# Kernel optimization log

Measured on AMD Instinct MI355X. Metric: run time of the kernel, lower is better.

The kernel has to match this reference:

```python
import jax, jax.numpy as jnp
import numpy as np


def setup_inputs() -> dict:
    key = jax.random.key(0)
    ks = jax.random.split(key, 6)
    B, Nu, Ni, D = 256, 512, 512, 64
    u_fea = jax.random.normal(ks[0], (B, Nu, D), dtype=jnp.float32)
    i_fea = jax.random.normal(ks[1], (B, Ni, D), dtype=jnp.float32)
    M = jax.random.normal(ks[2], (D, D), dtype=jnp.float32)
    # Linear weights, torch-style: y = x @ W.T + b (init scaled like torch default)
    lim = 1.0 / np.sqrt(D)
    Wu = jax.random.uniform(ks[3], (D, D), minval=-lim, maxval=lim, dtype=jnp.float32)
    Wi = jax.random.uniform(ks[4], (D, D), minval=-lim, maxval=lim, dtype=jnp.float32)
    bu = jnp.zeros((D,), dtype=jnp.float32)
    bi = jnp.zeros((D,), dtype=jnp.float32)
    return {"u_fea": u_fea, "i_fea": i_fea, "M": M, "Wu": Wu, "bu": bu, "Wi": Wi, "bi": bi}


def reference(u_fea, i_fea, M, Wu, bu, Wi, bi):
    # fc_u / fc_i: torch Linear is x @ W.T + b
    u = jnp.einsum('bud,ed->bue', u_fea, Wu) + bu   # [B, Nu, D]
    i = jnp.einsum('bid,ed->bie', i_fea, Wi) + bi   # [B, Ni, D]
    # Bilinear co-attention score S = u @ M @ i^T  -> [B, Nu, Ni]
    uM = jnp.einsum('bud,de->bue', u, M)
    S = jnp.einsum('bue,bie->bui', uM, i)
    # pooling == 'max'
    u_score = S.max(axis=2)   # [B, Nu]
    i_score = S.max(axis=1)   # [B, Ni]
    # gumbel == False -> plain softmax over the review axis
    p_u = jax.nn.softmax(u_score, axis=1)
    p_i = jax.nn.softmax(i_score, axis=1)
    return (p_u[:, :, None], p_i[:, :, None])
```

## Files before the change

kernel.cpp:

```cpp
#include <hip/hip_runtime.h>
#include <hip/hip_bf16.h>
#include <float.h>


#define NBATCH 256
#define NSEQ   512
#define DIM    64

typedef __attribute__((ext_vector_type(8))) short short8;
typedef __attribute__((ext_vector_type(4))) float f32x4;

#define MFMA16(a,b,c) __builtin_amdgcn_mfma_f32_16x16x32_bf16(a,b,c,0,0,0)

union BF2 { __hip_bfloat162 b; short2 s; };

__device__ __forceinline__ void cvt2(float f, unsigned short &h, unsigned short &l) {
    unsigned u = __float_as_uint(f);
    unsigned hb = (u + 0x7FFFu + ((u >> 16) & 1u)) >> 16;
    h = (unsigned short)hb;
    float r = f - __uint_as_float(hb << 16);
    unsigned u2 = __float_as_uint(r);
    l = (unsigned short)((u2 + 0x7FFFu + ((u2 >> 16) & 1u)) >> 16);
}

__device__ __forceinline__ void cvt8(const f32x4 a, const f32x4 b, short8 &hi, short8 &lo) {
    BF2 h0, h1, h2, h3;
    h0.b = __float22bfloat162_rn(make_float2(a[0], a[1]));
    h1.b = __float22bfloat162_rn(make_float2(a[2], a[3]));
    h2.b = __float22bfloat162_rn(make_float2(b[0], b[1]));
    h3.b = __float22bfloat162_rn(make_float2(b[2], b[3]));
    hi = short8{h0.s.x, h0.s.y, h1.s.x, h1.s.y, h2.s.x, h2.s.y, h3.s.x, h3.s.y};
    BF2 l0, l1, l2, l3;
    l0.b = __float22bfloat162_rn(make_float2(a[0] - __bfloat162float(h0.b.x),
                                             a[1] - __bfloat162float(h0.b.y)));
    l1.b = __float22bfloat162_rn(make_float2(a[2] - __bfloat162float(h1.b.x),
                                             a[3] - __bfloat162float(h1.b.y)));
    l2.b = __float22bfloat162_rn(make_float2(b[0] - __bfloat162float(h2.b.x),
                                             b[1] - __bfloat162float(h2.b.y)));
    l3.b = __float22bfloat162_rn(make_float2(b[2] - __bfloat162float(h3.b.x),
                                             b[3] - __bfloat162float(h3.b.y)));
    lo = short8{l0.s.x, l0.s.y, l1.s.x, l1.s.y, l2.s.x, l2.s.y, l3.s.x, l3.s.y};
}

__global__ __launch_bounds__(64) void coatt_prep1(
    const float* __restrict__ M, const float* __restrict__ Wi,
    const float* __restrict__ bi, float* __restrict__ ws)
{
    __shared__ float Ml[64];
    const int d = blockIdx.x, f = threadIdx.x;
    Ml[f] = M[d*64 + f];
    __syncthreads();
    float s = 0.f;
    #pragma unroll 8
    for (int e = 0; e < 64; ++e) s = fmaf(Ml[e], Wi[e*64 + f], s);
    ws[8448 + d*64 + f] = s;
    float p = Ml[f] * bi[f];
    #pragma unroll
    for (int off = 1; off < 64; off <<= 1) p += __shfl_xor(p, off, 64);
    if (f == 0) ws[12544 + d] = p;
}

__global__ __launch_bounds__(64) void coatt_prep2(
    const float* __restrict__ Wu, const float* __restrict__ bu,
    float* __restrict__ ws)
{
    __shared__ float col[64];
    const int c = blockIdx.x, f = threadIdx.x;
    const float* T = ws + 8448;
    col[f] = Wu[f*64 + c];
    __syncthreads();
    float s = 0.f;
    #pragma unroll 8
    for (int d = 0; d < 64; ++d) s = fmaf(col[d], T[d*64 + f], s);
    unsigned short* efh = (unsigned short*)(ws + 4352);
    unsigned short* efl = efh + 4096;
    unsigned short h, l;
    cvt2(s, h, l);
    const int ko = c >> 5, quad = (c >> 3) & 3, j = c & 7;
    const int ft = f >> 4, f15 = f & 15;
    const int p = ft*1024 + ko*512 + (quad*16 + f15)*8 + j;
    efh[p] = h; efl[p] = l;
    float pa = col[f] * ws[12544 + f];
    #pragma unroll
    for (int off = 1; off < 64; off <<= 1) pa += __shfl_xor(pa, off, 64);
    if (f == 0) ws[4096 + c] = pa;
    if (c == 0) {
        float sg = 0.f;
        #pragma unroll 8
        for (int d = 0; d < 64; ++d) sg = fmaf(bu[d], T[d*64 + f], sg);
        ws[4160 + f] = sg;
        float ps = bu[f] * ws[12544 + f];
        #pragma unroll
        for (int off = 1; off < 64; off <<= 1) ps += __shfl_xor(ps, off, 64);
        if (f == 0) ws[4224] = ps;
    }
}

#define LDS_BYTES 149568

__global__ __launch_bounds__(512, 2) void coatt_main(
    const float* __restrict__ u_fea, const float* __restrict__ i_fea,
    const float* __restrict__ ws, float* __restrict__ out)
{
    extern __shared__ char sm[];
    unsigned short* YH = (unsigned short*)sm;
    unsigned short* YL = (unsigned short*)(sm + 65536);
    float* colp   = (float*)(sm + 131072);
    float* uscore = (float*)(sm + 147456);
    float* red    = (float*)(sm + 149504);

    const int t    = threadIdx.x;
    const int lane = t & 63, w = t >> 6, quad = lane >> 4, l15 = lane & 15;
    const int b = blockIdx.x;
    const float* ub = u_fea + (size_t)b * NSEQ * DIM;
    const float* ib = i_fea + (size_t)b * NSEQ * DIM;

    const unsigned short* efh = (const unsigned short*)(ws + 4352);
    const unsigned short* efl = efh + 4096;
    short8 EH[4][2], EL[4][2];
    #pragma unroll
    for (int ft = 0; ft < 4; ++ft)
        #pragma unroll
        for (int ko = 0; ko < 2; ++ko) {
            EH[ft][ko] = *(const short8*)(efh + ((ft*2+ko)*64 + lane)*8);
            EL[ft][ko] = *(const short8*)(efl + ((ft*2+ko)*64 + lane)*8);
        }
    f32x4 gq[4];
    #pragma unroll
    for (int ft = 0; ft < 4; ++ft) gq[ft] = *(const f32x4*)(ws + 4160 + ft*16 + quad*4);
    const f32x4 av0 = *(const f32x4*)(ws + 4096 + quad*8);
    const f32x4 av1 = *(const f32x4*)(ws + 4096 + quad*8 + 4);
    const f32x4 av2 = *(const f32x4*)(ws + 4096 + 32 + quad*8);
    const f32x4 av3 = *(const f32x4*)(ws + 4096 + 32 + quad*8 + 4);
    const float s0 = ws[4224];

    #pragma unroll
    for (int bt = 0; bt < 2; ++bt) {
        f32x4 ya[4], yb[4];
        #pragma unroll
        for (int q = 0; q < 4; ++q) {
            const int task = bt*4 + q;
            const int tile = w*4 + (task >> 1);
            const int p = task & 1;
            const float* yp = ib + (size_t)(tile*16 + l15)*64 + p*16 + quad*4;
            ya[q] = *(const f32x4*)yp;
            yb[q] = *(const f32x4*)(yp + 32);
        }
        #pragma unroll
        for (int q = 0; q < 4; ++q) {
            const int task = bt*4 + q;
            const int tile = w*4 + (task >> 1);
            const int p = task & 1;
            short8 sh, sl;
            cvt8(ya[q], yb[q], sh, sl);
            const int off = tile*1024 + p*512 + lane*8;
            *(short8*)(YH + off) = sh;
            *(short8*)(YL + off) = sl;
        }
    }

    const int base = w*64;
    f32x4 u[4][4];
    #pragma unroll
    for (int g = 0; g < 4; ++g) {
        const float* up = ub + (size_t)(base + g*16 + l15)*64 + quad*8;
        u[g][0] = *(const f32x4*)up;
        u[g][1] = *(const f32x4*)(up + 4);
        u[g][2] = *(const f32x4*)(up + 32);
        u[g][3] = *(const f32x4*)(up + 36);
    }
    short8 XH[4][2], XL[4][2];
    f32x4 rv[4];
    #pragma unroll
    for (int g = 0; g < 4; ++g) {
        short8 UH0, UL0, UH1, UL1;
        cvt8(u[g][0], u[g][1], UH0, UL0);
        cvt8(u[g][2], u[g][3], UH1, UL1);
        float rp = 0.f;
        #pragma unroll
        for (int e = 0; e < 4; ++e) rp = fmaf(u[g][0][e], av0[e], rp);
        #pragma unroll
        for (int e = 0; e < 4; ++e) rp = fmaf(u[g][1][e], av1[e], rp);
        #pragma unroll
        for (int e = 0; e < 4; ++e) rp = fmaf(u[g][2][e], av2[e], rp);
        #pragma unroll
        for (int e = 0; e < 4; ++e) rp = fmaf(u[g][3][e], av3[e], rp);
        rp += __shfl_xor(rp, 16, 64);
        rp += __shfl_xor(rp, 32, 64);
        rp += s0;
        f32x4 ct[4];
        #pragma unroll
        for (int ft = 0; ft < 4; ++ft) {
            f32x4 c = gq[ft];
            c = MFMA16(EH[ft][0], UH0, c);
            c = MFMA16(EH[ft][1], UH1, c);
            c = MFMA16(EH[ft][0], UL0, c);
            c = MFMA16(EH[ft][1], UL1, c);
            c = MFMA16(EL[ft][0], UH0, c);
            c = MFMA16(EL[ft][1], UH1, c);
            ct[ft] = c;
        }
        cvt8(ct[0], ct[2], XH[g][0], XL[g][0]);
        cvt8(ct[1], ct[3], XH[g][1], XL[g][1]);
        #pragma unroll
        for (int rg = 0; rg < 4; ++rg)
            rv[g][rg] = __shfl(rp, quad*4 + rg, 64);
    }
    __syncthreads();

    f32x4 rm[4];
    #pragma unroll
    for (int g = 0; g < 4; ++g)
        rm[g] = (f32x4){-FLT_MAX, -FLT_MAX, -FLT_MAX, -FLT_MAX};
    for (int T = 0; T < 32; ++T) {
        const unsigned short* yh2 = YH + T*1024 + lane*8;
        const unsigned short* yl2 = YL + T*1024 + lane*8;
        const short8 BH0 = *(const short8*)(yh2);
        const short8 BH1 = *(const short8*)(yh2 + 512);
        const short8 BL0 = *(const short8*)(yl2);
        const short8 BL1 = *(const short8*)(yl2 + 512);
        float cg[4];
        #pragma unroll
        for (int g = 0; g < 4; ++g) {
            f32x4 c = rv[g];
            c = MFMA16(XH[g][0], BH0, c);
            c = MFMA16(XH[g][1], BH1, c);
            c = MFMA16(XH[g][0], BL0, c);
            c = MFMA16(XH[g][1], BL1, c);
            c = MFMA16(XL[g][0], BH0, c);
            c = MFMA16(XL[g][1], BH1, c);
            rm[g][0] = fmaxf(rm[g][0], c[0]);
            rm[g][1] = fmaxf(rm[g][1], c[1]);
            rm[g][2] = fmaxf(rm[g][2], c[2]);
            rm[g][3] = fmaxf(rm[g][3], c[3]);
            cg[g] = fmaxf(fmaxf(c[0], c[1]), fmaxf(c[2], c[3]));
        }
        float cm = fmaxf(fmaxf(cg[0], cg[1]), fmaxf(cg[2], cg[3]));
        cm = fmaxf(cm, __shfl_xor(cm, 16, 64));
        cm = fmaxf(cm, __shfl_xor(cm, 32, 64));
        if (lane < 16) colp[w*512 + T*16 + lane] = cm;
    }
    #pragma unroll
    for (int g = 0; g < 4; ++g)
        #pragma unroll
        for (int rg = 0; rg < 4; ++rg) {
            float v = rm[g][rg];
            v = fmaxf(v, __shfl_xor(v, 1, 64));
            v = fmaxf(v, __shfl_xor(v, 2, 64));
            v = fmaxf(v, __shfl_xor(v, 4, 64));
            v = fmaxf(v, __shfl_xor(v, 8, 64));
            if (l15 == 0) uscore[base + g*16 + quad*4 + rg] = v;
        }
    __syncthreads();

    {
        float v = uscore[t];
        float m = v;
        #pragma unroll
        for (int off = 1; off < 64; off <<= 1) m = fmaxf(m, __shfl_xor(m, off, 64));
        if (lane == 0) red[w] = m;
        __syncthreads();
        m = red[0];
        #pragma unroll
        for (int q = 1; q < 8; ++q) m = fmaxf(m, red[q]);
        const float e = __expf(v - m);
        float s = e;
        #pragma unroll
        for (int off = 1; off < 64; off <<= 1) s += __shfl_xor(s, off, 64);
        if (lane == 0) red[8+w] = s;
        __syncthreads();
        float sum = red[8];
        #pragma unroll
        for (int q = 1; q < 8; ++q) sum += red[8+q];
        out[(size_t)b*NSEQ + t] = e * (1.0f / sum);
    }
    __syncthreads();
    {
        float v = colp[t];
        #pragma unroll
        for (int s8 = 1; s8 < 8; ++s8) v = fmaxf(v, colp[s8*512 + t]);
        float m = v;
        #pragma unroll
        for (int off = 1; off < 64; off <<= 1) m = fmaxf(m, __shfl_xor(m, off, 64));
        if (lane == 0) red[w] = m;
        __syncthreads();
        m = red[0];
        #pragma unroll
        for (int q = 1; q < 8; ++q) m = fmaxf(m, red[q]);
        const float e = __expf(v - m);
        float s = e;
        #pragma unroll
        for (int off = 1; off < 64; off <<= 1) s += __shfl_xor(s, off, 64);
        if (lane == 0) red[8+w] = s;
        __syncthreads();
        float sum = red[8];
        #pragma unroll
        for (int q = 1; q < 8; ++q) sum += red[8+q];
        out[(size_t)NBATCH*NSEQ + (size_t)b*NSEQ + t] = e * (1.0f / sum);
    }
}

extern "C" void kernel_launch(void* const* d_in, const int* in_sizes, int n_in,
                              void* d_out, int out_size, void* d_ws, size_t ws_size,
                              hipStream_t stream) {
    const float* u_fea = (const float*)d_in[0];
    const float* i_fea = (const float*)d_in[1];
    const float* M     = (const float*)d_in[2];
    const float* Wu    = (const float*)d_in[3];
    const float* bu    = (const float*)d_in[4];
    const float* Wi    = (const float*)d_in[5];
    const float* bi    = (const float*)d_in[6];
    float* out = (float*)d_out;
    float* ws  = (float*)d_ws;

    coatt_prep1<<<64, 64, 0, stream>>>(M, Wi, bi, ws);
    coatt_prep2<<<64, 64, 0, stream>>>(Wu, bu, ws);
    coatt_main<<<NBATCH, 512, LDS_BYTES, stream>>>(u_fea, i_fea, ws, out);
}
```

Measured before the change: 140.4 us.

## Split each batch into 2x2 quadrant blocks and move softmax to an epilogue kernel

The main kernel now launches four blocks per batch, each covering half of the user rows and half of the item columns. This halves LDS use, allowing higher occupancy and four times as many blocks to fill the GPU. Partial row and column maxima are written to global buffers, and a new epilogue kernel merges them and computes both softmaxes. The MFMA accumulation chains are also split into two independent accumulators to cut dependency latency. In exchange, the u projection (the E-matrix MFMAs) is recomputed, each i tile is loaded twice, and there is one extra kernel launch plus global round-trips.

```diff
diff --git a/kernel.cpp b/kernel.cpp
--- a/kernel.cpp
+++ b/kernel.cpp
@@ -11,6 +11,9 @@
 typedef __attribute__((ext_vector_type(4))) float f32x4;
 
 #define MFMA16(a,b,c) __builtin_amdgcn_mfma_f32_16x16x32_bf16(a,b,c,0,0,0)
+
+__device__ float g_rmax[NBATCH*2*NSEQ];
+__device__ float g_cmax[NBATCH*2*NSEQ];
 
 union BF2 { __hip_bfloat162 b; short2 s; };
 
@@ -96,86 +99,60 @@
     }
 }
 
-#define LDS_BYTES 149568
-
-__global__ __launch_bounds__(512, 2) void coatt_main(
+#define LDS_BYTES 73728
+
+__global__ __launch_bounds__(512, 4) void coatt_main(
     const float* __restrict__ u_fea, const float* __restrict__ i_fea,
-    const float* __restrict__ ws, float* __restrict__ out)
+    const float* __restrict__ ws)
 {
     extern __shared__ char sm[];
     unsigned short* YH = (unsigned short*)sm;
-    unsigned short* YL = (unsigned short*)(sm + 65536);
-    float* colp   = (float*)(sm + 131072);
-    float* uscore = (float*)(sm + 147456);
-    float* red    = (float*)(sm + 149504);
+    unsigned short* YL = (unsigned short*)(sm + 32768);
+    float* colp = (float*)(sm + 65536);
 
     const int t    = threadIdx.x;
     const int lane = t & 63, w = t >> 6, quad = lane >> 4, l15 = lane & 15;
-    const int b = blockIdx.x;
+    const int bid = blockIdx.x;
+    const int b = bid >> 2, nh = (bid >> 1) & 1, mh = bid & 1;
     const float* ub = u_fea + (size_t)b * NSEQ * DIM;
     const float* ib = i_fea + (size_t)b * NSEQ * DIM;
 
-    const unsigned short* efh = (const unsigned short*)(ws + 4352);
-    const unsigned short* efl = efh + 4096;
-    short8 EH[4][2], EL[4][2];
-    #pragma unroll
-    for (int ft = 0; ft < 4; ++ft)
-        #pragma unroll
-        for (int ko = 0; ko < 2; ++ko) {
-            EH[ft][ko] = *(const short8*)(efh + ((ft*2+ko)*64 + lane)*8);
-            EL[ft][ko] = *(const short8*)(efl + ((ft*2+ko)*64 + lane)*8);
-        }
-    f32x4 gq[4];
-    #pragma unroll
-    for (int ft = 0; ft < 4; ++ft) gq[ft] = *(const f32x4*)(ws + 4160 + ft*16 + quad*4);
+    f32x4 ya[4], yb[4];
+    #pragma unroll
+    for (int q = 0; q < 4; ++q) {
+        const int tloc = w*2 + (q >> 1), p = q & 1;
+        const float* yp = ib + (size_t)(mh*256 + tloc*16 + l15)*DIM + p*16 + quad*4;
+        ya[q] = *(const f32x4*)yp;
+        yb[q] = *(const f32x4*)(yp + 32);
+    }
+    const int nbase = nh*256 + w*32;
+    f32x4 u[2][4];
+    #pragma unroll
+    for (int g = 0; g < 2; ++g) {
+        const float* up = ub + (size_t)(nbase + g*16 + l15)*DIM + quad*8;
+        u[g][0] = *(const f32x4*)up;
+        u[g][1] = *(const f32x4*)(up + 4);
+        u[g][2] = *(const f32x4*)(up + 32);
+        u[g][3] = *(const f32x4*)(up + 36);
+    }
+    #pragma unroll
+    for (int q = 0; q < 4; ++q) {
+        const int tloc = w*2 + (q >> 1), p = q & 1;
+        short8 sh, sl;
+        cvt8(ya[q], yb[q], sh, sl);
+        const int off = tloc*1024 + p*512 + lane*8;
+        *(short8*)(YH + off) = sh;
+        *(short8*)(YL + off) = sl;
+    }
     const f32x4 av0 = *(const f32x4*)(ws + 4096 + quad*8);
     const f32x4 av1 = *(const f32x4*)(ws + 4096 + quad*8 + 4);
     const f32x4 av2 = *(const f32x4*)(ws + 4096 + 32 + quad*8);
     const f32x4 av3 = *(const f32x4*)(ws + 4096 + 32 + quad*8 + 4);
     const float s0 = ws[4224];
-
-    #pragma unroll
-    for (int bt = 0; bt < 2; ++bt) {
-        f32x4 ya[4], yb[4];
-        #pragma unroll
-        for (int q = 0; q < 4; ++q) {
-            const int task = bt*4 + q;
-            const int tile = w*4 + (task >> 1);
-            const int p = task & 1;
-            const float* yp = ib + (size_t)(tile*16 + l15)*64 + p*16 + quad*4;
-            ya[q] = *(const f32x4*)yp;
-            yb[q] = *(const f32x4*)(yp + 32);
-        }
-        #pragma unroll
-        for (int q = 0; q < 4; ++q) {
-            const int task = bt*4 + q;
-            const int tile = w*4 + (task >> 1);
-            const int p = task & 1;
-            short8 sh, sl;
-            cvt8(ya[q], yb[q], sh, sl);
-            const int off = tile*1024 + p*512 + lane*8;
-            *(short8*)(YH + off) = sh;
-            *(short8*)(YL + off) = sl;
-        }
-    }
-
-    const int base = w*64;
-    f32x4 u[4][4];
-    #pragma unroll
-    for (int g = 0; g < 4; ++g) {
-        const float* up = ub + (size_t)(base + g*16 + l15)*64 + quad*8;
-        u[g][0] = *(const f32x4*)up;
-        u[g][1] = *(const f32x4*)(up + 4);
-        u[g][2] = *(const f32x4*)(up + 32);
-        u[g][3] = *(const f32x4*)(up + 36);
-    }
-    short8 XH[4][2], XL[4][2];
-    f32x4 rv[4];
-    #pragma unroll
-    for (int g = 0; g < 4; ++g) {
-        short8 UH0, UL0, UH1, UL1;
-        cvt8(u[g][0], u[g][1], UH0, UL0);
-        cvt8(u[g][2], u[g][3], UH1, UL1);
+    short8 UH[2][2], UL[2][2];
+    f32x4 rv[2];
+    #pragma unroll
+    for (int g = 0; g < 2; ++g) {
         float rp = 0.f;
         #pragma unroll
         for (int e = 0; e < 4; ++e) rp = fmaf(u[g][0][e], av0[e], rp);
@@ -188,60 +165,80 @@
         rp += __shfl_xor(rp, 16, 64);
         rp += __shfl_xor(rp, 32, 64);
         rp += s0;
-        f32x4 ct[4];
-        #pragma unroll
-        for (int ft = 0; ft < 4; ++ft) {
-            f32x4 c = gq[ft];
-            c = MFMA16(EH[ft][0], UH0, c);
-            c = MFMA16(EH[ft][1], UH1, c);
-            c = MFMA16(EH[ft][0], UL0, c);
-            c = MFMA16(EH[ft][1], UL1, c);
-            c = MFMA16(EL[ft][0], UH0, c);
-            c = MFMA16(EL[ft][1], UH1, c);
-            ct[ft] = c;
-        }
-        cvt8(ct[0], ct[2], XH[g][0], XL[g][0]);
-        cvt8(ct[1], ct[3], XH[g][1], XL[g][1]);
+        cvt8(u[g][0], u[g][1], UH[g][0], UL[g][0]);
+        cvt8(u[g][2], u[g][3], UH[g][1], UL[g][1]);
         #pragma unroll
         for (int rg = 0; rg < 4; ++rg)
             rv[g][rg] = __shfl(rp, quad*4 + rg, 64);
     }
-    __syncthreads();
-
-    f32x4 rm[4];
-    #pragma unroll
-    for (int g = 0; g < 4; ++g)
-        rm[g] = (f32x4){-FLT_MAX, -FLT_MAX, -FLT_MAX, -FLT_MAX};
-    for (int T = 0; T < 32; ++T) {
+    const unsigned short* efh = (const unsigned short*)(ws + 4352);
+    const unsigned short* efl = efh + 4096;
+    short8 XH[2][2], XL[2][2];
+    #pragma unroll
+    for (int p = 0; p < 2; ++p) {
+        f32x4 ct[2][2];
+        #pragma unroll
+        for (int fh = 0; fh < 2; ++fh) {
+            const int ft = p + fh*2;
+            const short8 Eh0 = *(const short8*)(efh + (ft*2+0)*512 + lane*8);
+            const short8 Eh1 = *(const short8*)(efh + (ft*2+1)*512 + lane*8);
+            const short8 El0 = *(const short8*)(efl + (ft*2+0)*512 + lane*8);
+            const short8 El1 = *(const short8*)(efl + (ft*2+1)*512 + lane*8);
+            const f32x4 gq = *(const f32x4*)(ws + 4160 + ft*16 + quad*4);
+            #pragma unroll
+            for (int g = 0; g < 2; ++g) {
+                f32x4 cA = gq;
+                cA = MFMA16(Eh0, UH[g][0], cA);
+                cA = MFMA16(Eh1, UH[g][1], cA);
+                cA = MFMA16(Eh0, UL[g][0], cA);
+                f32x4 cB = {0.f, 0.f, 0.f, 0.f};
+                cB = MFMA16(Eh1, UL[g][1], cB);
+                cB = MFMA16(El0, UH[g][0], cB);
+                cB = MFMA16(El1, UH[g][1], cB);
+                ct[g][fh] = cA + cB;
+            }
+        }
+        #pragma unroll
+        for (int g = 0; g < 2; ++g)
+            cvt8(ct[g][0], ct[g][1], XH[g][p], XL[g][p]);
+    }
+    __syncthreads();
+
+    f32x4 rm[2];
+    rm[0] = (f32x4){-FLT_MAX, -FLT_MAX, -FLT_MAX, -FLT_MAX};
+    rm[1] = rm[0];
+    for (int T = 0; T < 16; ++T) {
         const unsigned short* yh2 = YH + T*1024 + lane*8;
         const unsigned short* yl2 = YL + T*1024 + lane*8;
         const short8 BH0 = *(const short8*)(yh2);
         const short8 BH1 = *(const short8*)(yh2 + 512);
         const short8 BL0 = *(const short8*)(yl2);
         const short8 BL1 = *(const short8*)(yl2 + 512);
-        float cg[4];
-        #pragma unroll
-        for (int g = 0; g < 4; ++g) {
-            f32x4 c = rv[g];
-            c = MFMA16(XH[g][0], BH0, c);
-            c = MFMA16(XH[g][1], BH1, c);
-            c = MFMA16(XH[g][0], BL0, c);
-            c = MFMA16(XH[g][1], BL1, c);
-            c = MFMA16(XL[g][0], BH0, c);
-            c = MFMA16(XL[g][1], BH1, c);
+        float cg[2];
+        #pragma unroll
+        for (int g = 0; g < 2; ++g) {
+            f32x4 cA = rv[g];
+            cA = MFMA16(XH[g][0], BH0, cA);
+            cA = MFMA16(XH[g][1], BH1, cA);
+            cA = MFMA16(XH[g][0], BL0, cA);
+            f32x4 cB = {0.f, 0.f, 0.f, 0.f};
+            cB = MFMA16(XH[g][1], BL1, cB);
+            cB = MFMA16(XL[g][0], BH0, cB);
+            cB = MFMA16(XL[g][1], BH1, cB);
+            const f32x4 c = cA + cB;
             rm[g][0] = fmaxf(rm[g][0], c[0]);
             rm[g][1] = fmaxf(rm[g][1], c[1]);
             rm[g][2] = fmaxf(rm[g][2], c[2]);
             rm[g][3] = fmaxf(rm[g][3], c[3]);
             cg[g] = fmaxf(fmaxf(c[0], c[1]), fmaxf(c[2], c[3]));
         }
-        float cm = fmaxf(fmaxf(cg[0], cg[1]), fmaxf(cg[2], cg[3]));
+        float cm = fmaxf(cg[0], cg[1]);
         cm = fmaxf(cm, __shfl_xor(cm, 16, 64));
         cm = fmaxf(cm, __shfl_xor(cm, 32, 64));
-        if (lane < 16) colp[w*512 + T*16 + lane] = cm;
-    }
-    #pragma unroll
-    for (int g = 0; g < 4; ++g)
+        if (lane < 16) colp[w*256 + T*16 + lane] = cm;
+    }
+    #pragma unroll
+    for (int g = 0; g < 2; ++g)
         #pragma unroll
         for (int rg = 0; rg < 4; ++rg) {
             float v = rm[g][rg];
@@ -249,12 +246,25 @@
             v = fmaxf(v, __shfl_xor(v, 2, 64));
             v = fmaxf(v, __shfl_xor(v, 4, 64));
             v = fmaxf(v, __shfl_xor(v, 8, 64));
-            if (l15 == 0) uscore[base + g*16 + quad*4 + rg] = v;
+            if (l15 == 0)
+                g_rmax[(size_t)(b*2 + mh)*NSEQ + nbase + g*16 + quad*4 + rg] = v;
         }
     __syncthreads();
-
+    if (t < 256) {
+        float v = colp[t];
+        #pragma unroll
+        for (int s8 = 1; s8 < 8; ++s8) v = fmaxf(v, colp[s8*256 + t]);
+        g_cmax[(size_t)(b*2 + nh)*NSEQ + mh*256 + t] = v;
+    }
+}
+
+__global__ __launch_bounds__(512) void coatt_epi(float* __restrict__ out)
+{
+    __shared__ float red[16];
+    const int b = blockIdx.x, t = threadIdx.x, lane = t & 63, w = t >> 6;
     {
-        float v = uscore[t];
+        const float v = fmaxf(g_rmax[(size_t)(b*2+0)*NSEQ + t],
+                              g_rmax[(size_t)(b*2+1)*NSEQ + t]);
         float m = v;
         #pragma unroll
         for (int off = 1; off < 64; off <<= 1) m = fmaxf(m, __shfl_xor(m, off, 64));
@@ -276,9 +286,8 @@
     }
     __syncthreads();
     {
-        float v = colp[t];
-        #pragma unroll
-        for (int s8 = 1; s8 < 8; ++s8) v = fmaxf(v, colp[s8*512 + t]);
+        const float v = fmaxf(g_cmax[(size_t)(b*2+0)*NSEQ + t],
+                              g_cmax[(size_t)(b*2+1)*NSEQ + t]);
         float m = v;
         #pragma unroll
         for (int off = 1; off < 64; off <<= 1) m = fmaxf(m, __shfl_xor(m, off, 64));
@@ -315,5 +324,6 @@
 
     coatt_prep1<<<64, 64, 0, stream>>>(M, Wi, bi, ws);
     coatt_prep2<<<64, 64, 0, stream>>>(Wu, bu, ws);
-    coatt_main<<<NBATCH, 512, LDS_BYTES, stream>>>(u_fea, i_fea, ws, out);
-}
+    coatt_main<<<NBATCH*4, 512, LDS_BYTES, stream>>>(u_fea, i_fea, ws);
+    coatt_epi<<<NBATCH, 512, 0, stream>>>(out);
+}
```

Result: slower. 189.0 us (+34.6%).

## Merge prep kernels, halve LDS via two-pass i tiles and atomic column max

Applied to the files above, without the earlier changes.

Fuses the two weight-preparation kernels into one launch by recomputing the intermediate product inside each block. The main kernel now stages i_fea in two halves of 256 rows, cutting LDS from about 146KB to about 74KB. It replaces per-wave column-max buffers with four shared slices updated through atomicMax on an order-preserving integer encoding of floats. MFMA accumulation chains are split into two partial accumulators for more instruction-level parallelism. The costs are an extra barrier and a second load/convert phase between halves, plus LDS atomic contention.

```diff
diff --git a/kernel.cpp b/kernel.cpp
--- a/kernel.cpp
+++ b/kernel.cpp
@@ -13,6 +13,15 @@
 #define MFMA16(a,b,c) __builtin_amdgcn_mfma_f32_16x16x32_bf16(a,b,c,0,0,0)
 
 union BF2 { __hip_bfloat162 b; short2 s; };
+
+__device__ __forceinline__ unsigned fenc(float x) {
+    unsigned u = __float_as_uint(x);
+    return (u >> 31) ? ~u : (u | 0x80000000u);
+}
+__device__ __forceinline__ float fdec(unsigned m) {
+    unsigned u = (m >> 31) ? (m & 0x7FFFFFFFu) : ~m;
+    return __uint_as_float(u);
+}
 
 __device__ __forceinline__ void cvt2(float f, unsigned short &h, unsigned short &l) {
     unsigned u = __float_as_uint(f);
@@ -42,61 +51,55 @@
     lo = short8{l0.s.x, l0.s.y, l1.s.x, l1.s.y, l2.s.x, l2.s.y, l3.s.x, l3.s.y};
 }
 
-__global__ __launch_bounds__(64) void coatt_prep1(
-    const float* __restrict__ M, const float* __restrict__ Wi,
+__global__ __launch_bounds__(64) void coatt_prep(
+    const float* __restrict__ M, const float* __restrict__ Wu,
+    const float* __restrict__ bu, const float* __restrict__ Wi,
     const float* __restrict__ bi, float* __restrict__ ws)
 {
-    __shared__ float Ml[64];
-    const int d = blockIdx.x, f = threadIdx.x;
-    Ml[f] = M[d*64 + f];
+    __shared__ float Wucol[64];
+    __shared__ float Pc[64];
+    __shared__ float qv[64];
+    const int c = blockIdx.x, f = threadIdx.x;
+    Wucol[f] = Wu[f*64 + c];
     __syncthreads();
-    float s = 0.f;
+    float p = 0.f;
     #pragma unroll 8
-    for (int e = 0; e < 64; ++e) s = fmaf(Ml[e], Wi[e*64 + f], s);
-    ws[8448 + d*64 + f] = s;
-    float p = Ml[f] * bi[f];
-    #pragma unroll
-    for (int off = 1; off < 64; off <<= 1) p += __shfl_xor(p, off, 64);
-    if (f == 0) ws[12544 + d] = p;
-}
-
-__global__ __launch_bounds__(64) void coatt_prep2(
-    const float* __restrict__ Wu, const float* __restrict__ bu,
-    float* __restrict__ ws)
-{
-    __shared__ float col[64];
-    const int c = blockIdx.x, f = threadIdx.x;
-    const float* T = ws + 8448;
-    col[f] = Wu[f*64 + c];
+    for (int d = 0; d < 64; ++d) p = fmaf(Wucol[d], M[d*64 + f], p);
+    Pc[f] = p;
     __syncthreads();
-    float s = 0.f;
+    float e = 0.f;
     #pragma unroll 8
-    for (int d = 0; d < 64; ++d) s = fmaf(col[d], T[d*64 + f], s);
+    for (int k = 0; k < 64; ++k) e = fmaf(Pc[k], Wi[k*64 + f], e);
     unsigned short* efh = (unsigned short*)(ws + 4352);
     unsigned short* efl = efh + 4096;
     unsigned short h, l;
-    cvt2(s, h, l);
-    const int ko = c >> 5, quad = (c >> 3) & 3, j = c & 7;
+    cvt2(e, h, l);
+    const int ko = c >> 5, quadc = (c >> 3) & 3, j = c & 7;
     const int ft = f >> 4, f15 = f & 15;
-    const int p = ft*1024 + ko*512 + (quad*16 + f15)*8 + j;
-    efh[p] = h; efl[p] = l;
-    float pa = col[f] * ws[12544 + f];
+    const int pidx = ft*1024 + ko*512 + (quadc*16 + f15)*8 + j;
+    efh[pidx] = h; efl[pidx] = l;
+    float pa = Pc[f] * bi[f];
     #pragma unroll
     for (int off = 1; off < 64; off <<= 1) pa += __shfl_xor(pa, off, 64);
     if (f == 0) ws[4096 + c] = pa;
     if (c == 0) {
-        float sg = 0.f;
+        float q0 = 0.f;
         #pragma unroll 8
-        for (int d = 0; d < 64; ++d) sg = fmaf(bu[d], T[d*64 + f], sg);
-        ws[4160 + f] = sg;
-        float ps = bu[f] * ws[12544 + f];
+        for (int d = 0; d < 64; ++d) q0 = fmaf(bu[d], M[d*64 + f], q0);
+        qv[f] = q0;
+        __syncthreads();
+        float gg = 0.f;
+        #pragma unroll 8
+        for (int k = 0; k < 64; ++k) gg = fmaf(qv[k], Wi[k*64 + f], gg);
+        ws[4160 + f] = gg;
+        float ps = qv[f] * bi[f];
         #pragma unroll
         for (int off = 1; off < 64; off <<= 1) ps += __shfl_xor(ps, off, 64);
         if (f == 0) ws[4224] = ps;
     }
 }
 
-#define LDS_BYTES 149568
+#define LDS_BYTES 75840
 
 __global__ __launch_bounds__(512, 2) void coatt_main(
     const float* __restrict__ u_fea, const float* __restrict__ i_fea,
@@ -104,16 +107,19 @@
 {
     extern __shared__ char sm[];
     unsigned short* YH = (unsigned short*)sm;
-    unsigned short* YL = (unsigned short*)(sm + 65536);
-    float* colp   = (float*)(sm + 131072);
-    float* uscore = (float*)(sm + 147456);
-    float* red    = (float*)(sm + 149504);
+    unsigned short* YL = (unsigned short*)(sm + 32768);
+    unsigned* colp = (unsigned*)(sm + 65536);
+    float* uscore  = (float*)(sm + 73728);
+    float* red     = (float*)(sm + 75776);
 
     const int t    = threadIdx.x;
     const int lane = t & 63, w = t >> 6, quad = lane >> 4, l15 = lane & 15;
     const int b = blockIdx.x;
     const float* ub = u_fea + (size_t)b * NSEQ * DIM;
     const float* ib = i_fea + (size_t)b * NSEQ * DIM;
+
+    #pragma unroll
+    for (int i = 0; i < 4; ++i) colp[i*512 + t] = 0u;
 
     const unsigned short* efh = (const unsigned short*)(ws + 4352);
     const unsigned short* efl = efh + 4096;
@@ -135,70 +141,55 @@
     const float s0 = ws[4224];
 
     #pragma unroll
-    for (int bt = 0; bt < 2; ++bt) {
-        f32x4 ya[4], yb[4];
-        #pragma unroll
-        for (int q = 0; q < 4; ++q) {
-            const int task = bt*4 + q;
-            const int tile = w*4 + (task >> 1);
-            const int p = task & 1;
-            const float* yp = ib + (size_t)(tile*16 + l15)*64 + p*16 + quad*4;
-            ya[q] = *(const f32x4*)yp;
-            yb[q] = *(const f32x4*)(yp + 32);
-        }
-        #pragma unroll
-        for (int q = 0; q < 4; ++q) {
-            const int task = bt*4 + q;
-            const int tile = w*4 + (task >> 1);
-            const int p = task & 1;
-            short8 sh, sl;
-            cvt8(ya[q], yb[q], sh, sl);
-            const int off = tile*1024 + p*512 + lane*8;
-            *(short8*)(YH + off) = sh;
-            *(short8*)(YL + off) = sl;
-        }
+    for (int q = 0; q < 4; ++q) {
+        const int tl = w*2 + (q >> 1), p = q & 1;
+        const float* yp = ib + (size_t)(tl*16 + l15)*DIM + p*16 + quad*4;
+        const f32x4 a0 = *(const f32x4*)yp;
+        const f32x4 b0 = *(const f32x4*)(yp + 32);
+        short8 sh, sl;
+        cvt8(a0, b0, sh, sl);
+        const int off = tl*1024 + p*512 + lane*8;
+        *(short8*)(YH + off) = sh;
+        *(short8*)(YL + off) = sl;
     }
 
     const int base = w*64;
-    f32x4 u[4][4];
-    #pragma unroll
-    for (int g = 0; g < 4; ++g) {
-        const float* up = ub + (size_t)(base + g*16 + l15)*64 + quad*8;
-        u[g][0] = *(const f32x4*)up;
-        u[g][1] = *(const f32x4*)(up + 4);
-        u[g][2] = *(const f32x4*)(up + 32);
-        u[g][3] = *(const f32x4*)(up + 36);
-    }
     short8 XH[4][2], XL[4][2];
     f32x4 rv[4];
     #pragma unroll
     for (int g = 0; g < 4; ++g) {
-        short8 UH0, UL0, UH1, UL1;
-        cvt8(u[g][0], u[g][1], UH0, UL0);
-        cvt8(u[g][2], u[g][3], UH1, UL1);
+        const float* up = ub + (size_t)(base + g*16 + l15)*DIM + quad*8;
+        const f32x4 u0 = *(const f32x4*)up;
+        const f32x4 u1 = *(const f32x4*)(up + 4);
+        const f32x4 u2 = *(const f32x4*)(up + 32);
+        const f32x4 u3 = *(const f32x4*)(up + 36);
         float rp = 0.f;
         #pragma unroll
-        for (int e = 0; e < 4; ++e) rp = fmaf(u[g][0][e], av0[e], rp);
-        #pragma unroll
-        for (int e = 0; e < 4; ++e) rp = fmaf(u[g][1][e], av1[e], rp);
-        #pragma unroll
-        for (int e = 0; e < 4; ++e) rp = fmaf(u[g][2][e], av2[e], rp);
-        #pragma unroll
-        for (int e = 0; e < 4; ++e) rp = fmaf(u[g][3][e], av3[e], rp);
+        for (int e = 0; e < 4; ++e) rp = fmaf(u0[e], av0[e], rp);
+        #pragma unroll
+        for (int e = 0; e < 4; ++e) rp = fmaf(u1[e], av1[e], rp);
+        #pragma unroll
+        for (int e = 0; e < 4; ++e) rp = fmaf(u2[e], av2[e], rp);
+        #pragma unroll
+        for (int e = 0; e < 4; ++e) rp = fmaf(u3[e], av3[e], rp);
         rp += __shfl_xor(rp, 16, 64);
         rp += __shfl_xor(rp, 32, 64);
         rp += s0;
+        short8 UH0, UL0, UH1, UL1;
+        cvt8(u0, u1, UH0, UL0);
+        cvt8(u2, u3, UH1, UL1);
         f32x4 ct[4];
         #pragma unroll
         for (int ft = 0; ft < 4; ++ft) {
-            f32x4 c = gq[ft];
-            c = MFMA16(EH[ft][0], UH0, c);
-            c = MFMA16(EH[ft][1], UH1, c);
-            c = MFMA16(EH[ft][0], UL0, c);
-            c = MFMA16(EH[ft][1], UL1, c);
-            c = MFMA16(EL[ft][0], UH0, c);
-            c = MFMA16(EL[ft][1], UH1, c);
-            ct[ft] = c;
+            f32x4 cA = gq[ft];
+            cA = MFMA16(EH[ft][0], UH0, cA);
+            cA = MFMA16(EH[ft][1], UH1, cA);
+            cA = MFMA16(EH[ft][0], UL0, cA);
+            f32x4 cB = {0.f, 0.f, 0.f, 0.f};
+            cB = MFMA16(EH[ft][1], UL1, cB);
+            cB = MFMA16(EL[ft][0], UH0, cB);
+            cB = MFMA16(EL[ft][1], UH1, cB);
+            ct[ft] = cA + cB;
         }
         cvt8(ct[0], ct[2], XH[g][0], XL[g][0]);
         cvt8(ct[1], ct[3], XH[g][1], XL[g][1]);
@@ -206,40 +197,65 @@
         for (int rg = 0; rg < 4; ++rg)
             rv[g][rg] = __shfl(rp, quad*4 + rg, 64);
     }
-    __syncthreads();
 
     f32x4 rm[4];
     #pragma unroll
     for (int g = 0; g < 4; ++g)
         rm[g] = (f32x4){-FLT_MAX, -FLT_MAX, -FLT_MAX, -FLT_MAX};
-    for (int T = 0; T < 32; ++T) {
-        const unsigned short* yh2 = YH + T*1024 + lane*8;
-        const unsigned short* yl2 = YL + T*1024 + lane*8;
-        const short8 BH0 = *(const short8*)(yh2);
-        const short8 BH1 = *(const short8*)(yh2 + 512);
-        const short8 BL0 = *(const short8*)(yl2);
-        const short8 BL1 = *(const short8*)(yl2 + 512);
-        float cg[4];
-        #pragma unroll
-        for (int g = 0; g < 4; ++g) {
-            f32x4 c = rv[g];
-            c = MFMA16(XH[g][0], BH0, c);
-            c = MFMA16(XH[g][1], BH1, c);
-            c = MFMA16(XH[g][0], BL0, c);
-            c = MFMA16(XH[g][1], BL1, c);
-            c = MFMA16(XL[g][0], BH0, c);
-            c = MFMA16(XL[g][1], BH1, c);
-            rm[g][0] = fmaxf(rm[g][0], c[0]);
-            rm[g][1] = fmaxf(rm[g][1], c[1]);
-            rm[g][2] = fmaxf(rm[g][2], c[2]);
-            rm[g][3] = fmaxf(rm[g][3], c[3]);
-            cg[g] = fmaxf(fmaxf(c[0], c[1]), fmaxf(c[2], c[3]));
-        }
-        float cm = fmaxf(fmaxf(cg[0], cg[1]), fmaxf(cg[2], cg[3]));
-        cm = fmaxf(cm, __shfl_xor(cm, 16, 64));
-        cm = fmaxf(cm, __shfl_xor(cm, 32, 64));
-        if (lane < 16) colp[w*512 + T*16 + lane] = cm;
-    }
+    const int slice = (w & 3) * 512;
+
+    #pragma unroll
+    for (int h = 0; h < 2; ++h) {
+        if (h == 1) {
+            __syncthreads();
+            #pragma unroll
+            for (int q = 0; q < 4; ++q) {
+                const int tl = w*2 + (q >> 1), p = q & 1;
+                const float* yp = ib + (size_t)(256 + tl*16 + l15)*DIM + p*16 + quad*4;
+                const f32x4 a0 = *(const f32x4*)yp;
+                const f32x4 b0 = *(const f32x4*)(yp + 32);
+                short8 sh, sl;
+                cvt8(a0, b0, sh, sl);
+                const int off = tl*1024 + p*512 + lane*8;
+                *(short8*)(YH + off) = sh;
+                *(short8*)(YL + off) = sl;
+            }
+        }
+        __syncthreads();
+
+        for (int T = 0; T < 16; ++T) {
+            const unsigned short* yh2 = YH + T*1024 + lane*8;
+            const unsigned short* yl2 = YL + T*1024 + lane*8;
+            const short8 BH0 = *(const short8*)(yh2);
+            const short8 BH1 = *(const short8*)(yh2 + 512);
+            const short8 BL0 = *(const short8*)(yl2);
+            const short8 BL1 = *(const short8*)(yl2 + 512);
+            float cg[4];
+            #pragma unroll
+            for (int g = 0; g < 4; ++g) {
+                f32x4 cA = rv[g];
+                cA = MFMA16(XH[g][0], BH0, cA);
+                cA = MFMA16(XH[g][1], BH1, cA);
+                cA = MFMA16(XH[g][0], BL0, cA);
+                f32x4 cB = {0.f, 0.f, 0.f, 0.f};
+                cB = MFMA16(XH[g][1], BL1, cB);
+                cB = MFMA16(XL[g][0], BH0, cB);
+                cB = MFMA16(XL[g][1], BH1, cB);
+                const f32x4 c = cA + cB;
+                rm[g][0] = fmaxf(rm[g][0], c[0]);
+                rm[g][1] = fmaxf(rm[g][1], c[1]);
+                rm[g][2] = fmaxf(rm[g][2], c[2]);
+                rm[g][3] = fmaxf(rm[g][3], c[3]);
+                cg[g] = fmaxf(fmaxf(c[0], c[1]), fmaxf(c[2], c[3]));
+            }
+            float cm = fmaxf(fmaxf(cg[0], cg[1]), fmaxf(cg[2], cg[3]));
+            cm = fmaxf(cm, __shfl_xor(cm, 16, 64));
+            cm = fmaxf(cm, __shfl_xor(cm, 32, 64));
+            if (lane < 16)
+                atomicMax(&colp[slice + h*256 + T*16 + lane], fenc(cm));
+        }
+    }
+
     #pragma unroll
     for (int g = 0; g < 4; ++g)
         #pragma unroll
@@ -254,7 +270,7 @@
     __syncthreads();
 
     {
-        float v = uscore[t];
+        const float v = uscore[t];
         float m = v;
         #pragma unroll
         for (int off = 1; off < 64; off <<= 1) m = fmaxf(m, __shfl_xor(m, off, 64));
@@ -276,9 +292,10 @@
     }
     __syncthreads();
     {
-        float v = colp[t];
-        #pragma unroll
-        for (int s8 = 1; s8 < 8; ++s8) v = fmaxf(v, colp[s8*512 + t]);
+        float v = fdec(colp[t]);
+        v = fmaxf(v, fdec(colp[512 + t]));
+        v = fmaxf(v, fdec(colp[1024 + t]));
+        v = fmaxf(v, fdec(colp[1536 + t]));
         float m = v;
         #pragma unroll
         for (int off = 1; off < 64; off <<= 1) m = fmaxf(m, __shfl_xor(m, off, 64));
@@ -313,7 +330,6 @@
     float* out = (float*)d_out;
     float* ws  = (float*)d_ws;
 
-    coatt_prep1<<<64, 64, 0, stream>>>(M, Wi, bi, ws);
-    coatt_prep2<<<64, 64, 0, stream>>>(Wu, bu, ws);
+    coatt_prep<<<64, 64, 0, stream>>>(M, Wu, bu, Wi, bi, ws);
     coatt_main<<<NBATCH, 512, LDS_BYTES, stream>>>(u_fea, i_fea, ws, out);
 }
```

Result: slower. 197.6 us (+40.7%).
